# Optimization experiments

Measured on AMD Instinct MI355X. Metric: run time of the kernel, lower is better.

The kernel has to match this reference:

```python
import jax, jax.numpy as jnp
import numpy as np

Np_, Ny, Nu = 5, 8, 4
NZ = Np_ * (Ny + Nu)  # 60


def setup_inputs() -> dict:
    key = jax.random.key(0)
    ks = jax.random.split(key, 6)
    B, T = 8192, 1024
    u = jax.random.normal(ks[0], (B, T, Nu), dtype=jnp.float32)
    z0 = jax.random.normal(ks[1], (B, NZ), dtype=jnp.float32)
    W1 = jax.random.normal(ks[2], (NZ, 128), dtype=jnp.float32) * (1.0 / np.sqrt(NZ))
    b1 = jnp.zeros((128,), dtype=jnp.float32)
    W2 = jax.random.normal(ks[3], (128, 128), dtype=jnp.float32) * (1.0 / np.sqrt(128))
    b2 = jnp.zeros((128,), dtype=jnp.float32)
    W3 = jax.random.normal(ks[4], (128, Ny), dtype=jnp.float32) * (1.0 / np.sqrt(128))
    b3 = jnp.zeros((Ny,), dtype=jnp.float32)
    return {"u": u, "z0": z0, "W1": W1, "b1": b1, "W2": W2, "b2": b2,
            "W3": W3, "b3": b3}


def reference(u, z0, W1, b1, W2, b2, W3, b3):
    # u: [B, T, Nu], z0: [B, Np*(Ny+Nu)] -> y sequence [B, T, Ny]
    def step(z, u_t):
        h = jnp.tanh(z @ W1 + b1)
        h = jnp.tanh(h @ W2 + b2)
        y = h @ W3 + b3                      # [B, Ny]
        ypseq = z[:, : Np_ * Ny]
        upseq = z[:, Np_ * Ny:]
        z_new = jnp.concatenate(
            (ypseq[:, Ny:], y, upseq[:, Nu:], u_t), axis=-1)
        return z_new, y

    u_tbc = jnp.transpose(u, (1, 0, 2))      # [T, B, Nu]
    _, ys = jax.lax.scan(step, z0, u_tbc)    # ys: [T, B, Ny]
    return jnp.transpose(ys, (1, 0, 2))      # [B, T, Ny]
```

## Files before the change

### kernel.cpp

```cpp
#include <hip/hip_runtime.h>

#define T_STEPS 1024
#define NZV 60
#define H 128
#define NY 8
#define NU 4
#define ZSTR 72
#define HSTR 136

typedef __attribute__((ext_vector_type(8))) short bf16x8;
typedef __attribute__((ext_vector_type(4))) short bf16x4;
typedef __attribute__((ext_vector_type(4))) float f32x4;
typedef __attribute__((ext_vector_type(2))) unsigned uint2v;

union U4 { unsigned u[4]; bf16x8 v; };
union U2 { unsigned u[2]; bf16x4 v; };

__device__ __forceinline__ unsigned short f2bf(float x) {
    unsigned u = __float_as_uint(x);
    u += 0x7FFFu + ((u >> 16) & 1u);
    return (unsigned short)(u >> 16);
}

__device__ __forceinline__ unsigned cvt_pk_bf16(float lo, float hi) {
    unsigned r;
    asm("v_cvt_pk_bf16_f32 %0, %1, %2" : "=v"(r) : "v"(lo), "v"(hi));
    return r;
}

__device__ __forceinline__ float tanh_fast(float x) {
    float e = __builtin_amdgcn_exp2f(x * 2.8853900817779268f);
    return fmaf(-2.0f, __builtin_amdgcn_rcpf(e + 1.0f), 1.0f);
}

#define MFMA32 __builtin_amdgcn_mfma_f32_16x16x32_bf16

__device__ __forceinline__ f32x4 gemm3_pair(bf16x4 a0, bf16x4 b0,
                                            bf16x4 a1, bf16x4 b1, f32x4 c) {
    asm("s_nop 1\n\t"
        "v_mfma_f32_16x16x16_bf16 %0, %1, %2, %0\n\t"
        "v_mfma_f32_16x16x16_bf16 %0, %3, %4, %0\n\t"
        "s_nop 7\n\t"
        "s_nop 7"
        : "+v"(c) : "v"(a0), "v"(b0), "v"(a1), "v"(b1));
    return c;
}

__global__ __launch_bounds__(256, 2)
void cstr_scan_kernel(const float* __restrict__ u_g, const float* __restrict__ z0_g,
                      const float* __restrict__ W1, const float* __restrict__ b1,
                      const float* __restrict__ W2, const float* __restrict__ b2,
                      const float* __restrict__ W3, const float* __restrict__ b3,
                      float* __restrict__ out) {
    __shared__ unsigned short zbuf[2][16][ZSTR];
    __shared__ unsigned short h1s[16][HSTR];
    __shared__ f32x4 ypart[4][64];
    __shared__ float ybuf[32][16][NY];
    __shared__ float ubuf[2][16][16][NU];

    const int tid   = threadIdx.x;
    const int wid   = tid >> 6;
    const int lane  = tid & 63;
    const int b0    = blockIdx.x * 16;
    const int col   = lane & 15;
    const int kg    = lane >> 4;
    const int urow  = lane >> 2;
    const int uc    = lane & 3;
    const int nbase = wid * 32;
    const int frow  = tid >> 4;
    const int ftoff = tid & 15;

    bf16x8 w1f[2][2], w2f[4][2];
    bf16x4 w3a0, w3a1;
    f32x4 b1t[2], b2t[2], b3t;
#pragma unroll
    for (int nl = 0; nl < 2; ++nl)
#pragma unroll
        for (int r = 0; r < 4; ++r) {
            b1t[nl][r] = b1[nbase + nl * 16 + kg * 4 + r];
            b2t[nl][r] = b2[nbase + nl * 16 + kg * 4 + r];
        }
#pragma unroll
    for (int r = 0; r < 4; ++r) {
        int m = kg * 4 + r;
        b3t[r] = (m < NY) ? b3[m] : 0.f;
    }
#pragma unroll
    for (int kc = 0; kc < 2; ++kc)
#pragma unroll
        for (int nl = 0; nl < 2; ++nl) {
            bf16x8 v;
#pragma unroll
            for (int j = 0; j < 8; ++j) {
                int k = kc * 32 + kg * 8 + j;
                float w = (k < NZV) ? W1[k * H + nbase + nl * 16 + col] : 0.f;
                v[j] = (short)f2bf(w);
            }
            w1f[kc][nl] = v;
        }
#pragma unroll
    for (int kc = 0; kc < 4; ++kc)
#pragma unroll
        for (int nl = 0; nl < 2; ++nl) {
            bf16x8 v;
#pragma unroll
            for (int j = 0; j < 8; ++j) {
                int k = kc * 32 + kg * 8 + j;
                v[j] = (short)f2bf(W2[k * H + nbase + nl * 16 + col]);
            }
            w2f[kc][nl] = v;
        }
    {
        bf16x4 v0, v1;
#pragma unroll
        for (int j = 0; j < 4; ++j) {
            v0[j] = (short)f2bf((col < NY) ? W3[(nbase + 0  + kg * 4 + j) * NY + col] : 0.f);
            v1[j] = (short)f2bf((col < NY) ? W3[(nbase + 16 + kg * 4 + j) * NY + col] : 0.f);
        }
        w3a0 = v0; w3a1 = v1;
    }

#define LOAD_UWIN(BI, T0)                                                              \
    if (wid == 1) {                                                                    \
        const float* usrc = u_g + (size_t)(b0 + (lane & 15)) * (T_STEPS * NU)          \
                            + (size_t)((T0) + (lane >> 4)) * NU;                       \
        _Pragma("unroll")                                                              \
        for (int k_ = 0; k_ < 4; ++k_)                                                 \
            __builtin_amdgcn_global_load_lds(                                          \
                (const __attribute__((address_space(1))) unsigned*)(usrc + k_ * 16),   \
                (__attribute__((address_space(3))) unsigned*)(&ubuf[BI][k_ * 4][0][0]),\
                16, 0, 0);                                                             \
    }

    {
        unsigned short* zs = &zbuf[0][0][0];
        for (int i = tid; i < 2 * 16 * ZSTR; i += 256) zs[i] = 0;
        __syncthreads();
        for (int i = tid; i < 16 * NZV; i += 256) {
            int r = i / NZV, c = i - r * NZV;
            zbuf[0][r][c] = f2bf(z0_g[(size_t)(b0 + r) * NZV + c]);
        }
        LOAD_UWIN(0, 0)
        __syncthreads();
    }

    bf16x8 za0, za1l;
    int t = 0;

    {
        bf16x8 pza0 = *(const bf16x8*)&zbuf[0][col][kg * 8];
        bf16x8 pza1 = *(const bf16x8*)&zbuf[0][col][32 + kg * 8];
#pragma unroll
        for (int nl = 0; nl < 2; ++nl) {
            f32x4 c1 = b1t[nl];
            c1 = MFMA32(w1f[0][nl], pza0, c1, 0, 0, 0);
            c1 = MFMA32(w1f[1][nl], pza1, c1, 0, 0, 0);
            unsigned p01 = cvt_pk_bf16(tanh_fast(c1[0]), tanh_fast(c1[1]));
            unsigned p23 = cvt_pk_bf16(tanh_fast(c1[2]), tanh_fast(c1[3]));
            *(uint2v*)&h1s[col][nbase + nl * 16 + kg * 4] = uint2v{p01, p23};
        }
        if (wid == 3) {
            bf16x4 m0 = *(const bf16x4*)&zbuf[0][urow][8 + 8 * uc];
            bf16x4 m1 = *(const bf16x4*)&zbuf[0][urow][12 + 8 * uc];
            bf16x4 m2 = *(const bf16x4*)&zbuf[0][urow][44 + 4 * uc];
            *(bf16x4*)&zbuf[1][urow][8 * uc]      = m0;
            *(bf16x4*)&zbuf[1][urow][8 * uc + 4]  = m1;
            *(bf16x4*)&zbuf[1][urow][40 + 4 * uc] = m2;
            zbuf[1][urow][56 + uc] = f2bf(ubuf[0][0][urow][uc]);
        }
        __syncthreads();
        bf16x8 ha0 = *(const bf16x8*)&h1s[col][0 * 32 + kg * 8];
        bf16x8 ha1 = *(const bf16x8*)&h1s[col][1 * 32 + kg * 8];
        bf16x8 ha2 = *(const bf16x8*)&h1s[col][2 * 32 + kg * 8];
        bf16x8 ha3 = *(const bf16x8*)&h1s[col][3 * 32 + kg * 8];
        za0  = *(const bf16x8*)&zbuf[1][col][kg * 8];
        za1l = *(const bf16x8*)&zbuf[1][col][32 + kg * 8];
        bf16x4 pb0, pb1;
#pragma unroll
        for (int nl = 0; nl < 2; ++nl) {
            f32x4 a0 = b2t[nl];
            f32x4 a1 = { 0.f, 0.f, 0.f, 0.f };
            a0 = MFMA32(w2f[0][nl], ha0, a0, 0, 0, 0);
            a1 = MFMA32(w2f[1][nl], ha1, a1, 0, 0, 0);
            a0 = MFMA32(w2f[2][nl], ha2, a0, 0, 0, 0);
            a1 = MFMA32(w2f[3][nl], ha3, a1, 0, 0, 0);
            f32x4 c2 = a0 + a1;
            U2 p; p.u[0] = cvt_pk_bf16(tanh_fast(c2[0]), tanh_fast(c2[1]));
            p.u[1]       = cvt_pk_bf16(tanh_fast(c2[2]), tanh_fast(c2[3]));
            if (nl == 0) pb0 = p.v; else pb1 = p.v;
        }
        f32x4 yp = (wid == 0) ? b3t : f32x4{0.f, 0.f, 0.f, 0.f};
        yp = gemm3_pair(w3a0, pb0, w3a1, pb1, yp);
        ypart[wid][lane] = yp;
        __syncthreads();
        t = 1;
    }

#define BODY(P)                                                                         \
    {                                                                                   \
                  \
        f32x4 y_ = ypart[0][lane] + ypart[1][lane] + ypart[2][lane] + ypart[3][lane];   \
        unsigned d0 = cvt_pk_bf16(y_[0], y_[1]);                                        \
        unsigned d1 = cvt_pk_bf16(y_[2], y_[3]);                                        \
        unsigned o0 = (unsigned)__builtin_amdgcn_ds_swizzle((int)d0, 0x401F);           \
        unsigned o1 = (unsigned)__builtin_amdgcn_ds_swizzle((int)d1, 0x401F);           \
        U4 zb_; zb_.u[0] = d0; zb_.u[1] = d1; zb_.u[2] = o0; zb_.u[3] = o1;             \
        bf16x8 za1 = (kg == 0) ? zb_.v : za1l;      \
        if (wid == 1 && kg < 2) {                                                       \
            *(f32x4*)&ybuf[(t - 1) & 31][col][kg * 4] = y_;                             \
            *(uint2v*)&zbuf[(P) ^ 1][col][24 + kg * 4] = uint2v{d0, d1};                \
        }                                                                               \
        _Pragma("unroll")                                                               \
        for (int nl = 0; nl < 2; ++nl) {                                                \
            f32x4 c1 = b1t[nl];                                                         \
            c1 = MFMA32(w1f[0][nl], za0, c1, 0, 0, 0);                                  \
            c1 = MFMA32(w1f[1][nl], za1, c1, 0, 0, 0);                                  \
            unsigned p01 = cvt_pk_bf16(tanh_fast(c1[0]), tanh_fast(c1[1]));             \
            unsigned p23 = cvt_pk_bf16(tanh_fast(c1[2]), tanh_fast(c1[3]));             \
            *(uint2v*)&h1s[col][nbase + nl * 16 + kg * 4] = uint2v{p01, p23};           \
        }                                                                               \
        if (wid == 3) {    \
            if (uc < 3) {                                                               \
                bf16x4 m0 = *(const bf16x4*)&zbuf[P][urow][8 + 8 * uc];                 \
                bf16x4 m1 = *(const bf16x4*)&zbuf[P][urow][12 + 8 * uc];                \
                *(bf16x4*)&zbuf[(P) ^ 1][urow][8 * uc]     = m0;                        \
                *(bf16x4*)&zbuf[(P) ^ 1][urow][8 * uc + 4] = m1;                        \
            }                                                                           \
            bf16x4 m2 = *(const bf16x4*)&zbuf[P][urow][44 + 4 * uc];                    \
            *(bf16x4*)&zbuf[(P) ^ 1][urow][40 + 4 * uc] = m2;                           \
            zbuf[(P) ^ 1][urow][56 + uc] = f2bf(ubuf[(t >> 4) & 1][t & 15][urow][uc]);  \
        }                                                                               \
        __syncthreads();                          \
        bf16x8 ha0 = *(const bf16x8*)&h1s[col][0 * 32 + kg * 8];                        \
        bf16x8 ha1 = *(const bf16x8*)&h1s[col][1 * 32 + kg * 8];                        \
        bf16x8 ha2 = *(const bf16x8*)&h1s[col][2 * 32 + kg * 8];                        \
        bf16x8 ha3 = *(const bf16x8*)&h1s[col][3 * 32 + kg * 8];                        \
        za0  = *(const bf16x8*)&zbuf[(P) ^ 1][col][kg * 8];            \
        za1l = *(const bf16x8*)&zbuf[(P) ^ 1][col][32 + kg * 8];                        \
        bf16x4 pb0, pb1;                                                                \
        _Pragma("unroll")                                                               \
        for (int nl = 0; nl < 2; ++nl) {                                                \
            f32x4 a0 = b2t[nl];                                                         \
            f32x4 a1 = { 0.f, 0.f, 0.f, 0.f };                                          \
            a0 = MFMA32(w2f[0][nl], ha0, a0, 0, 0, 0);                                  \
            a1 = MFMA32(w2f[1][nl], ha1, a1, 0, 0, 0);                                  \
            a0 = MFMA32(w2f[2][nl], ha2, a0, 0, 0, 0);                                  \
            a1 = MFMA32(w2f[3][nl], ha3, a1, 0, 0, 0);                                  \
            f32x4 c2 = a0 + a1;                                                         \
            U2 p; p.u[0] = cvt_pk_bf16(tanh_fast(c2[0]), tanh_fast(c2[1]));             \
            p.u[1]       = cvt_pk_bf16(tanh_fast(c2[2]), tanh_fast(c2[3]));             \
            if (nl == 0) pb0 = p.v; else pb1 = p.v;                                     \
        }                                                                               \
        f32x4 yp = (wid == 0) ? b3t : f32x4{0.f, 0.f, 0.f, 0.f};                        \
        yp = gemm3_pair(w3a0, pb0, w3a1, pb1, yp);                                      \
        ypart[wid][lane] = yp;                                                          \
        __syncthreads();                             \
        ++t;                                                                            \
    }

#define FLUSH(BT)                                                                       \
    {                                                                                   \
        const f32x4* yp_ = (const f32x4*)&ybuf[((BT) & 31) + ftoff][frow][0];           \
        f32x4 v0 = yp_[0], v1 = yp_[1];                                                 \
        float* op = out + ((size_t)(b0 + frow) * T_STEPS + (BT) + ftoff) * NY;          \
        *(f32x4*)op = v0;                                                               \
        *(f32x4*)(op + 4) = v1;                                                         \
    }

#pragma unroll 1
    for (int it = 0; it < 511; ++it) {
        if ((t & 15) == 1) {
            if (t > 1)
                FLUSH(t - 17)
            if (t + 15 < T_STEPS)
                LOAD_UWIN((((t + 15) >> 4) & 1), t + 15)
        }
        BODY(1)
        BODY(0)
    }
    BODY(1)
#undef BODY

    {
        f32x4 y_ = ypart[0][lane] + ypart[1][lane] + ypart[2][lane] + ypart[3][lane];
        if (wid == 1 && kg < 2)
            *(f32x4*)&ybuf[31][col][kg * 4] = y_;
        __syncthreads();
        const f32x4* yp_ = (const f32x4*)&ybuf[16 + ftoff][frow][0];
        f32x4 v0 = yp_[0], v1 = yp_[1];
        float* op = out + ((size_t)(b0 + frow) * T_STEPS + 1008 + ftoff) * NY;
        *(f32x4*)op = v0;
        *(f32x4*)(op + 4) = v1;
    }
#undef FLUSH
#undef LOAD_UWIN
}

extern "C" void kernel_launch(void* const* d_in, const int* in_sizes, int n_in,
                              void* d_out, int out_size, void* d_ws, size_t ws_size,
                              hipStream_t stream) {
    (void)in_sizes; (void)n_in; (void)d_ws; (void)ws_size; (void)out_size;
    const float* u  = (const float*)d_in[0];
    const float* z0 = (const float*)d_in[1];
    const float* W1 = (const float*)d_in[2];
    const float* b1 = (const float*)d_in[3];
    const float* W2 = (const float*)d_in[4];
    const float* b2 = (const float*)d_in[5];
    const float* W3 = (const float*)d_in[6];
    const float* b3 = (const float*)d_in[7];
    float* out = (float*)d_out;

    dim3 grid(8192 / 16);
    dim3 block(256);
    cstr_scan_kernel<<<grid, block, 0, stream>>>(u, z0, W1, b1, W2, b2, W3, b3, out);
}
```

Measured before the change: 979.0 us.

## Split hidden dimension across eight waves per block instead of four

Each block now runs 512 threads (8 wavefronts), with each wave owning 16 hidden columns instead of 32. Per-wave MFMA and tanh work per timestep is halved, and the y partial-sum reduction grows to eight partials. The aim is to shorten the serial critical path of each recurrent step by spreading it across more waves. In exchange, the per-step barrier now synchronises more waves, the reduction has more LDS reads, and the launch bounds are raised.

```diff
diff --git a/kernel.cpp b/kernel.cpp
--- a/kernel.cpp
+++ b/kernel.cpp
@@ -28,6 +28,10 @@
     return r;
 }
 
+__device__ __forceinline__ unsigned swz16(unsigned v) {
+    return (unsigned)__builtin_amdgcn_ds_swizzle((int)v, 0x401F);
+}
+
 __device__ __forceinline__ float tanh_fast(float x) {
     float e = __builtin_amdgcn_exp2f(x * 2.8853900817779268f);
     return fmaf(-2.0f, __builtin_amdgcn_rcpf(e + 1.0f), 1.0f);
@@ -35,18 +39,16 @@
 
 #define MFMA32 __builtin_amdgcn_mfma_f32_16x16x32_bf16
 
-__device__ __forceinline__ f32x4 gemm3_pair(bf16x4 a0, bf16x4 b0,
-                                            bf16x4 a1, bf16x4 b1, f32x4 c) {
+__device__ __forceinline__ f32x4 gemm3_one(bf16x4 a, bf16x4 b, f32x4 c) {
     asm("s_nop 1\n\t"
         "v_mfma_f32_16x16x16_bf16 %0, %1, %2, %0\n\t"
-        "v_mfma_f32_16x16x16_bf16 %0, %3, %4, %0\n\t"
         "s_nop 7\n\t"
         "s_nop 7"
-        : "+v"(c) : "v"(a0), "v"(b0), "v"(a1), "v"(b1));
+        : "+v"(c) : "v"(a), "v"(b));
     return c;
 }
 
-__global__ __launch_bounds__(256, 2)
+__global__ __launch_bounds__(512, 4)
 void cstr_scan_kernel(const float* __restrict__ u_g, const float* __restrict__ z0_g,
                       const float* __restrict__ W1, const float* __restrict__ b1,
                       const float* __restrict__ W2, const float* __restrict__ b2,
@@ -54,7 +56,7 @@
                       float* __restrict__ out) {
     __shared__ unsigned short zbuf[2][16][ZSTR];
     __shared__ unsigned short h1s[16][HSTR];
-    __shared__ f32x4 ypart[4][64];
+    __shared__ f32x4 ypart[8][32];
     __shared__ float ybuf[32][16][NY];
     __shared__ float ubuf[2][16][16][NU];
 
@@ -66,58 +68,46 @@
     const int kg    = lane >> 4;
     const int urow  = lane >> 2;
     const int uc    = lane & 3;
-    const int nbase = wid * 32;
+    const int nbase = wid * 16;
     const int frow  = tid >> 4;
     const int ftoff = tid & 15;
 
-    bf16x8 w1f[2][2], w2f[4][2];
-    bf16x4 w3a0, w3a1;
-    f32x4 b1t[2], b2t[2], b3t;
-#pragma unroll
-    for (int nl = 0; nl < 2; ++nl)
-#pragma unroll
-        for (int r = 0; r < 4; ++r) {
-            b1t[nl][r] = b1[nbase + nl * 16 + kg * 4 + r];
-            b2t[nl][r] = b2[nbase + nl * 16 + kg * 4 + r];
-        }
+    bf16x8 w1f[2], w2f[4];
+    bf16x4 w3a;
+    f32x4 b1t, b2t, b3t;
 #pragma unroll
     for (int r = 0; r < 4; ++r) {
-        int m = kg * 4 + r;
-        b3t[r] = (m < NY) ? b3[m] : 0.f;
-    }
-#pragma unroll
-    for (int kc = 0; kc < 2; ++kc)
-#pragma unroll
-        for (int nl = 0; nl < 2; ++nl) {
-            bf16x8 v;
-#pragma unroll
-            for (int j = 0; j < 8; ++j) {
-                int k = kc * 32 + kg * 8 + j;
-                float w = (k < NZV) ? W1[k * H + nbase + nl * 16 + col] : 0.f;
-                v[j] = (short)f2bf(w);
-            }
-            w1f[kc][nl] = v;
-        }
-#pragma unroll
-    for (int kc = 0; kc < 4; ++kc)
-#pragma unroll
-        for (int nl = 0; nl < 2; ++nl) {
-            bf16x8 v;
-#pragma unroll
-            for (int j = 0; j < 8; ++j) {
-                int k = kc * 32 + kg * 8 + j;
-                v[j] = (short)f2bf(W2[k * H + nbase + nl * 16 + col]);
-            }
-            w2f[kc][nl] = v;
-        }
+        b1t[r] = b1[nbase + kg * 4 + r];
+        b2t[r] = b2[nbase + kg * 4 + r];
+        b3t[r] = (wid == 0 && kg * 4 + r < NY) ? b3[kg * 4 + r] : 0.f;
+    }
+#pragma unroll
+    for (int kc = 0; kc < 2; ++kc) {
+        bf16x8 v;
+#pragma unroll
+        for (int j = 0; j < 8; ++j) {
+            int k = kc * 32 + kg * 8 + j;
+            float w = (k < NZV) ? W1[k * H + nbase + col] : 0.f;
+            v[j] = (short)f2bf(w);
+        }
+        w1f[kc] = v;
+    }
+#pragma unroll
+    for (int kc = 0; kc < 4; ++kc) {
+        bf16x8 v;
+#pragma unroll
+        for (int j = 0; j < 8; ++j) {
+            int k = kc * 32 + kg * 8 + j;
+            v[j] = (short)f2bf(W2[k * H + nbase + col]);
+        }
+        w2f[kc] = v;
+    }
     {
-        bf16x4 v0, v1;
-#pragma unroll
-        for (int j = 0; j < 4; ++j) {
-            v0[j] = (short)f2bf((col < NY) ? W3[(nbase + 0  + kg * 4 + j) * NY + col] : 0.f);
-            v1[j] = (short)f2bf((col < NY) ? W3[(nbase + 16 + kg * 4 + j) * NY + col] : 0.f);
-        }
-        w3a0 = v0; w3a1 = v1;
+        bf16x4 v;
+#pragma unroll
+        for (int j = 0; j < 4; ++j)
+            v[j] = (short)f2bf((col < NY) ? W3[(nbase + kg * 4 + j) * NY + col] : 0.f);
+        w3a = v;
     }
 
 #define LOAD_UWIN(BI, T0)                                                              \
@@ -134,9 +124,9 @@
 
     {
         unsigned short* zs = &zbuf[0][0][0];
-        for (int i = tid; i < 2 * 16 * ZSTR; i += 256) zs[i] = 0;
-        __syncthreads();
-        for (int i = tid; i < 16 * NZV; i += 256) {
+        for (int i = tid; i < 2 * 16 * ZSTR; i += 512) zs[i] = 0;
+        __syncthreads();
+        for (int i = tid; i < 16 * NZV; i += 512) {
             int r = i / NZV, c = i - r * NZV;
             zbuf[0][r][c] = f2bf(z0_g[(size_t)(b0 + r) * NZV + c]);
         }
@@ -150,16 +140,13 @@
     {
         bf16x8 pza0 = *(const bf16x8*)&zbuf[0][col][kg * 8];
         bf16x8 pza1 = *(const bf16x8*)&zbuf[0][col][32 + kg * 8];
-#pragma unroll
-        for (int nl = 0; nl < 2; ++nl) {
-            f32x4 c1 = b1t[nl];
-            c1 = MFMA32(w1f[0][nl], pza0, c1, 0, 0, 0);
-            c1 = MFMA32(w1f[1][nl], pza1, c1, 0, 0, 0);
-            unsigned p01 = cvt_pk_bf16(tanh_fast(c1[0]), tanh_fast(c1[1]));
-            unsigned p23 = cvt_pk_bf16(tanh_fast(c1[2]), tanh_fast(c1[3]));
-            *(uint2v*)&h1s[col][nbase + nl * 16 + kg * 4] = uint2v{p01, p23};
-        }
-        if (wid == 3) {
+        f32x4 c1 = b1t;
+        c1 = MFMA32(w1f[0], pza0, c1, 0, 0, 0);
+        c1 = MFMA32(w1f[1], pza1, c1, 0, 0, 0);
+        unsigned p01 = cvt_pk_bf16(tanh_fast(c1[0]), tanh_fast(c1[1]));
+        unsigned p23 = cvt_pk_bf16(tanh_fast(c1[2]), tanh_fast(c1[3]));
+        *(uint2v*)&h1s[col][nbase + kg * 4] = uint2v{p01, p23};
+        if (wid == 7) {
             bf16x4 m0 = *(const bf16x4*)&zbuf[0][urow][8 + 8 * uc];
             bf16x4 m1 = *(const bf16x4*)&zbuf[0][urow][12 + 8 * uc];
             bf16x4 m2 = *(const bf16x4*)&zbuf[0][urow][44 + 4 * uc];
@@ -175,51 +162,49 @@
         bf16x8 ha3 = *(const bf16x8*)&h1s[col][3 * 32 + kg * 8];
         za0  = *(const bf16x8*)&zbuf[1][col][kg * 8];
         za1l = *(const bf16x8*)&zbuf[1][col][32 + kg * 8];
-        bf16x4 pb0, pb1;
-#pragma unroll
-        for (int nl = 0; nl < 2; ++nl) {
-            f32x4 a0 = b2t[nl];
-            f32x4 a1 = { 0.f, 0.f, 0.f, 0.f };
-            a0 = MFMA32(w2f[0][nl], ha0, a0, 0, 0, 0);
-            a1 = MFMA32(w2f[1][nl], ha1, a1, 0, 0, 0);
-            a0 = MFMA32(w2f[2][nl], ha2, a0, 0, 0, 0);
-            a1 = MFMA32(w2f[3][nl], ha3, a1, 0, 0, 0);
-            f32x4 c2 = a0 + a1;
-            U2 p; p.u[0] = cvt_pk_bf16(tanh_fast(c2[0]), tanh_fast(c2[1]));
-            p.u[1]       = cvt_pk_bf16(tanh_fast(c2[2]), tanh_fast(c2[3]));
-            if (nl == 0) pb0 = p.v; else pb1 = p.v;
-        }
+        f32x4 a0 = b2t;
+        f32x4 a1 = { 0.f, 0.f, 0.f, 0.f };
+        a0 = MFMA32(w2f[0], ha0, a0, 0, 0, 0);
+        a1 = MFMA32(w2f[1], ha1, a1, 0, 0, 0);
+        a0 = MFMA32(w2f[2], ha2, a0, 0, 0, 0);
+        a1 = MFMA32(w2f[3], ha3, a1, 0, 0, 0);
+        f32x4 c2 = a0 + a1;
+        U2 p; p.u[0] = cvt_pk_bf16(tanh_fast(c2[0]), tanh_fast(c2[1]));
+        p.u[1]       = cvt_pk_bf16(tanh_fast(c2[2]), tanh_fast(c2[3]));
         f32x4 yp = (wid == 0) ? b3t : f32x4{0.f, 0.f, 0.f, 0.f};
-        yp = gemm3_pair(w3a0, pb0, w3a1, pb1, yp);
-        ypart[wid][lane] = yp;
+        yp = gemm3_one(w3a, p.v, yp);
+        if (kg < 2) ypart[wid][lane] = yp;
         __syncthreads();
         t = 1;
     }
 
 #define BODY(P)                                                                         \
     {                                                                                   \
-                  \
-        f32x4 y_ = ypart[0][lane] + ypart[1][lane] + ypart[2][lane] + ypart[3][lane];   \
-        unsigned d0 = cvt_pk_bf16(y_[0], y_[1]);                                        \
-        unsigned d1 = cvt_pk_bf16(y_[2], y_[3]);                                        \
-        unsigned o0 = (unsigned)__builtin_amdgcn_ds_swizzle((int)d0, 0x401F);           \
-        unsigned o1 = (unsigned)__builtin_amdgcn_ds_swizzle((int)d1, 0x401F);           \
+                        \
+        f32x4 y_ = { 0.f, 0.f, 0.f, 0.f };                                              \
+        unsigned d0 = 0, d1 = 0;                                                        \
+        if (kg < 2) {                                                                   \
+            y_ = ypart[0][lane] + ypart[1][lane] + ypart[2][lane] + ypart[3][lane]      \
+               + ypart[4][lane] + ypart[5][lane] + ypart[6][lane] + ypart[7][lane];     \
+            d0 = cvt_pk_bf16(y_[0], y_[1]);                                             \
+            d1 = cvt_pk_bf16(y_[2], y_[3]);                                             \
+        }                                                                               \
+        unsigned o0 = swz16(d0);                                                        \
+        unsigned o1 = swz16(d1);                                                        \
         U4 zb_; zb_.u[0] = d0; zb_.u[1] = d1; zb_.u[2] = o0; zb_.u[3] = o1;             \
         bf16x8 za1 = (kg == 0) ? zb_.v : za1l;      \
         if (wid == 1 && kg < 2) {                                                       \
             *(f32x4*)&ybuf[(t - 1) & 31][col][kg * 4] = y_;                             \
             *(uint2v*)&zbuf[(P) ^ 1][col][24 + kg * 4] = uint2v{d0, d1};                \
         }                                                                               \
-        _Pragma("unroll")                                                               \
-        for (int nl = 0; nl < 2; ++nl) {                                                \
-            f32x4 c1 = b1t[nl];                                                         \
-            c1 = MFMA32(w1f[0][nl], za0, c1, 0, 0, 0);                                  \
-            c1 = MFMA32(w1f[1][nl], za1, c1, 0, 0, 0);                                  \
-            unsigned p01 = cvt_pk_bf16(tanh_fast(c1[0]), tanh_fast(c1[1]));             \
-            unsigned p23 = cvt_pk_bf16(tanh_fast(c1[2]), tanh_fast(c1[3]));             \
-            *(uint2v*)&h1s[col][nbase + nl * 16 + kg * 4] = uint2v{p01, p23};           \
-        }                                                                               \
-        if (wid == 3) {    \
+                                                      \
+        f32x4 c1 = b1t;                                                                 \
+        c1 = MFMA32(w1f[0], za0, c1, 0, 0, 0);                                          \
+        c1 = MFMA32(w1f[1], za1, c1, 0, 0, 0);                                          \
+        unsigned p01 = cvt_pk_bf16(tanh_fast(c1[0]), tanh_fast(c1[1]));                 \
+        unsigned p23 = cvt_pk_bf16(tanh_fast(c1[2]), tanh_fast(c1[3]));                 \
+        *(uint2v*)&h1s[col][nbase + kg * 4] = uint2v{p01, p23};                         \
+        if (wid == 7) {    \
             if (uc < 3) {                                                               \
                 bf16x4 m0 = *(const bf16x4*)&zbuf[P][urow][8 + 8 * uc];                 \
                 bf16x4 m1 = *(const bf16x4*)&zbuf[P][urow][12 + 8 * uc];                \
@@ -237,29 +222,24 @@
         bf16x8 ha3 = *(const bf16x8*)&h1s[col][3 * 32 + kg * 8];                        \
         za0  = *(const bf16x8*)&zbuf[(P) ^ 1][col][kg * 8];            \
         za1l = *(const bf16x8*)&zbuf[(P) ^ 1][col][32 + kg * 8];                        \
-        bf16x4 pb0, pb1;                                                                \
-        _Pragma("unroll")                                                               \
-        for (int nl = 0; nl < 2; ++nl) {                                                \
-            f32x4 a0 = b2t[nl];                                                         \
-            f32x4 a1 = { 0.f, 0.f, 0.f, 0.f };                                          \
-            a0 = MFMA32(w2f[0][nl], ha0, a0, 0, 0, 0);                                  \
-            a1 = MFMA32(w2f[1][nl], ha1, a1, 0, 0, 0);                                  \
-            a0 = MFMA32(w2f[2][nl], ha2, a0, 0, 0, 0);                                  \
-            a1 = MFMA32(w2f[3][nl], ha3, a1, 0, 0, 0);                                  \
-            f32x4 c2 = a0 + a1;                                                         \
-            U2 p; p.u[0] = cvt_pk_bf16(tanh_fast(c2[0]), tanh_fast(c2[1]));             \
-            p.u[1]       = cvt_pk_bf16(tanh_fast(c2[2]), tanh_fast(c2[3]));             \
-            if (nl == 0) pb0 = p.v; else pb1 = p.v;                                     \
-        }                                                                               \
+        f32x4 a0 = b2t;                                                                 \
+        f32x4 a1 = { 0.f, 0.f, 0.f, 0.f };                                              \
+        a0 = MFMA32(w2f[0], ha0, a0, 0, 0, 0);                                          \
+        a1 = MFMA32(w2f[1], ha1, a1, 0, 0, 0);                                          \
+        a0 = MFMA32(w2f[2], ha2, a0, 0, 0, 0);                                          \
+        a1 = MFMA32(w2f[3], ha3, a1, 0, 0, 0);                                          \
+        f32x4 c2 = a0 + a1;                                                             \
+        U2 p; p.u[0] = cvt_pk_bf16(tanh_fast(c2[0]), tanh_fast(c2[1]));                 \
+        p.u[1]       = cvt_pk_bf16(tanh_fast(c2[2]), tanh_fast(c2[3]));                 \
         f32x4 yp = (wid == 0) ? b3t : f32x4{0.f, 0.f, 0.f, 0.f};                        \
-        yp = gemm3_pair(w3a0, pb0, w3a1, pb1, yp);                                      \
-        ypart[wid][lane] = yp;                                                          \
+        yp = gemm3_one(w3a, p.v, yp);                                                   \
+        if (kg < 2) ypart[wid][lane] = yp;                                              \
         __syncthreads();                             \
         ++t;                                                                            \
     }
 
 #define FLUSH(BT)                                                                       \
-    {                                                                                   \
+    if (tid < 256) {                                                                    \
         const f32x4* yp_ = (const f32x4*)&ybuf[((BT) & 31) + ftoff][frow][0];           \
         f32x4 v0 = yp_[0], v1 = yp_[1];                                                 \
         float* op = out + ((size_t)(b0 + frow) * T_STEPS + (BT) + ftoff) * NY;          \
@@ -282,15 +262,20 @@
 #undef BODY
 
     {
-        f32x4 y_ = ypart[0][lane] + ypart[1][lane] + ypart[2][lane] + ypart[3][lane];
-        if (wid == 1 && kg < 2)
-            *(f32x4*)&ybuf[31][col][kg * 4] = y_;
-        __syncthreads();
-        const f32x4* yp_ = (const f32x4*)&ybuf[16 + ftoff][frow][0];
-        f32x4 v0 = yp_[0], v1 = yp_[1];
-        float* op = out + ((size_t)(b0 + frow) * T_STEPS + 1008 + ftoff) * NY;
-        *(f32x4*)op = v0;
-        *(f32x4*)(op + 4) = v1;
+        if (kg < 2) {
+            f32x4 y_ = ypart[0][lane] + ypart[1][lane] + ypart[2][lane] + ypart[3][lane]
+                     + ypart[4][lane] + ypart[5][lane] + ypart[6][lane] + ypart[7][lane];
+            if (wid == 1)
+                *(f32x4*)&ybuf[31][col][kg * 4] = y_;
+        }
+        __syncthreads();
+        if (tid < 256) {
+            const f32x4* yp_ = (const f32x4*)&ybuf[16 + ftoff][frow][0];
+            f32x4 v0 = yp_[0], v1 = yp_[1];
+            float* op = out + ((size_t)(b0 + frow) * T_STEPS + 1008 + ftoff) * NY;
+            *(f32x4*)op = v0;
+            *(f32x4*)(op + 4) = v1;
+        }
     }
 #undef FLUSH
 #undef LOAD_UWIN
@@ -311,6 +296,6 @@
     float* out = (float*)d_out;
 
     dim3 grid(8192 / 16);
-    dim3 block(256);
+    dim3 block(512);
     cstr_scan_kernel<<<grid, block, 0, stream>>>(u, z0, W1, b1, W2, b2, W3, b3, out);
 }
```

After: 1.223 ms. 24.9% more time.
